# Optimization experiments

Hardware: AMD Instinct MI355X
Metric: run time of the kernel (lower is better)

Reference implementation:

```python
import jax, jax.numpy as jnp
import numpy as np

B, D, T = 16, 512, 2048
K, C = 8, 1024          # num_codebooks, codebook_size
CH = D // K             # chunk_size = 64
COMMIT = 0.25
EPS = 1e-8


def setup_inputs() -> dict:
    key = jax.random.key(0)
    k1, k2 = jax.random.split(key)
    x = jax.random.normal(k1, (B, D, T), dtype=jnp.float32)
    # kaiming-uniform-ish init for codebooks [K, C, CH]
    bound = float(np.sqrt(6.0 / CH))
    codebooks = jax.random.uniform(k2, (K, C, CH), dtype=jnp.float32,
                                   minval=-bound, maxval=bound)
    return {"x": x, "codebooks": codebooks}


def reference(x, codebooks):
    b, d, t = x.shape
    xc = x.reshape(b, K, CH, t)                       # [B,K,CH,T]
    x_norm = jnp.sum(xc * xc, axis=2)[:, :, None, :]  # [B,K,1,T]
    c_norm = jnp.sum(codebooks * codebooks, axis=2)[None, :, :, None]  # [1,K,C,1]
    cross = -2.0 * jnp.einsum('bkdt,kcd->bkct', xc, codebooks)         # [B,K,C,T]
    distances = x_norm + c_norm + cross
    indices = jnp.argmin(distances, axis=2)           # [B,K,T] int
    # gather nearest codewords -> [B,K,T,CH] -> [B,K,CH,T]
    q = codebooks[jnp.arange(K)[None, :, None], indices]
    q = jnp.transpose(q, (0, 1, 3, 2))                # [B,K,CH,T]
    # per-codebook usage histogram
    kk = jnp.broadcast_to(jnp.arange(K)[None, :, None], indices.shape)
    counts = jnp.zeros((K, C), dtype=jnp.float32).at[kk.ravel(), indices.ravel()].add(1.0)
    avg_probs = counts / (b * t)
    perplexity = jnp.exp(jnp.sum(-avg_probs * jnp.log(avg_probs + EPS), axis=1))
    # commitment losses
    sg = jax.lax.stop_gradient
    codebook_loss = jnp.mean((sg(xc) - q) ** 2)
    encoder_loss = jnp.mean((xc - sg(q)) ** 2)
    commit_loss = codebook_loss + COMMIT * encoder_loss
    # straight-through estimator
    quantized = xc + sg(q - xc)
    return quantized.reshape(b, d, t), commit_loss, perplexity
```

## Files before the change

kernel.cpp:

```cpp
#include <hip/hip_runtime.h>
#include <hip/hip_bf16.h>
#include <math.h>

#define B_   16
#define D_   512
#define T_   2048
#define K_   8
#define C_   1024
#define CH_  64
#define NEL_ (B_ * D_ * T_)
#define QOFF 16777216

#define WS_HCN   0
#define WS_CNT   32768
#define WS_SSE   65536
#define WS_CBS   66048

typedef __attribute__((ext_vector_type(8))) short   short8;
typedef __attribute__((ext_vector_type(8))) __bf16  bf16x8;
typedef __attribute__((ext_vector_type(4))) float   f32x4;

__device__ __forceinline__ unsigned short f2bf_rne(float f) {
    unsigned u = __builtin_bit_cast(unsigned, f);
    u = u + 0x7FFFu + ((u >> 16) & 1u);
    return (unsigned short)(u >> 16);
}

__device__ __forceinline__ void gload_lds16(const void* gsrc, void* ldst) {
    __builtin_amdgcn_global_load_lds(
        (const __attribute__((address_space(1))) unsigned int*)gsrc,
        (__attribute__((address_space(3))) unsigned int*)ldst,
        16, 0, 0);
}

__global__ void vq_prep(const float* __restrict__ cb,
                        unsigned char* __restrict__ cbS,
                        float* __restrict__ hcn,
                        int* __restrict__ counts,
                        double* __restrict__ sse) {
    int g   = blockIdx.x * 256 + threadIdx.x;
    if (g < K_ * C_) counts[g] = 0;
    if (g == 0) *sse = 0.0;

    int row = g >> 3;
    int s8  = g & 7;
    const float* src = cb + (size_t)row * CH_;

    short8 val;
#pragma unroll
    for (int j = 0; j < 8; ++j)
        val[j] = (short)f2bf_rne(-src[s8 * 8 + j]);
    *(short8*)(cbS + (size_t)row * 128 + ((s8 ^ (row & 7)) * 16)) = val;

    if (s8 == 0) {
        float s = 0.f;
#pragma unroll 8
        for (int ch = 0; ch < CH_; ++ch) {
            float v = src[ch];
            s = fmaf(v, v, s);
        }
        hcn[row] = 0.5f * s;
    }
}

#define LDSBUF 8192

__global__ __launch_bounds__(256, 8) void vq_main(
    const float* __restrict__ x,
    const float* __restrict__ cb,
    const unsigned char* __restrict__ cbS,
    const float* __restrict__ hcn,
    float* __restrict__ out,
    int* __restrict__ counts,
    double* __restrict__ sse)
{
    __shared__ __align__(16) unsigned char lds[2 * LDSBUF + 512];
    int* idxS = (int*)(lds + 2 * LDSBUF);

    const int tid  = threadIdx.x;
    const int lane = tid & 63;
    const int wave = tid >> 6;
    const int ln   = lane & 15;
    const int q    = lane >> 4;
    const int q4   = q * 4;

    const int bid = blockIdx.x;
    const int tc  = bid & 15;
    const int k   = (bid >> 4) & 7;
    const int b   = bid >> 7;
    const int t0  = tc * 128;
    const int tw  = t0 + wave * 32;

    short8 bh[2][2];
    float  xn[2];
#pragma unroll
    for (int tt = 0; tt < 2; ++tt) {
        int t = tw + tt * 16 + ln;
        float pn = 0.f;
#pragma unroll
        for (int ks = 0; ks < 2; ++ks) {
            const float* xp = x + ((size_t)(b * D_ + k * CH_ + ks * 32 + q * 8)) * T_ + t;
            short8 sh;
#pragma unroll
            for (int j = 0; j < 8; ++j) {
                float v = xp[(size_t)j * T_];
                pn = fmaf(v, v, pn);
                sh[j] = (short)f2bf_rne(v);
            }
            bh[tt][ks] = sh;
        }
        pn += __shfl_xor(pn, 16);
        pn += __shfl_xor(pn, 32);
        xn[tt] = pn;
    }

    const unsigned char* cbS_k = cbS + (size_t)k * C_ * 128;
    const float*         hcn_k = hcn + k * C_;

    {
        const unsigned char* src = cbS_k + tid * 16;
        unsigned char* dst = lds + tid * 16;
        gload_lds16(src,        dst);
        gload_lds16(src + 4096, dst + 4096);
    }

    float    md[2][4];
    unsigned mjp[2];
#pragma unroll
    for (int tt = 0; tt < 2; ++tt) {
        mjp[tt] = 0u;
#pragma unroll
        for (int r = 0; r < 4; ++r) md[tt][r] = INFINITY;
    }

    for (int chunk = 0; chunk < 16; ++chunk) {
        __syncthreads();

        if (chunk < 15) {
            const unsigned char* src = cbS_k + (size_t)(chunk + 1) * 8192 + tid * 16;
            unsigned char* dst = lds + ((chunk + 1) & 1) * LDSBUF + tid * 16;
            gload_lds16(src,        dst);
            gload_lds16(src + 4096, dst + 4096);
        }

        const unsigned char* buf = lds + (chunk & 1) * LDSBUF;
#pragma unroll
        for (int sub = 0; sub < 4; ++sub) {
            const unsigned char* rowb = buf + (sub * 16 + ln) * 128;
            f32x4 h4 = *(const f32x4*)(hcn_k + chunk * 64 + sub * 16 + q4);
            f32x4 a[2];
            a[0] = h4;
            a[1] = h4;
#pragma unroll
            for (int ks = 0; ks < 2; ++ks) {
                int cidx = ((ks * 4 + q) ^ (ln & 7)) * 16;
                bf16x8 ah = __builtin_bit_cast(bf16x8, *(const short8*)(rowb + cidx));
#pragma unroll
                for (int tt = 0; tt < 2; ++tt)
                    a[tt] = __builtin_amdgcn_mfma_f32_16x16x32_bf16(
                        ah, __builtin_bit_cast(bf16x8, bh[tt][ks]), a[tt], 0, 0, 0);
            }
            const unsigned j = (unsigned)(chunk * 4 + sub);
#pragma unroll
            for (int tt = 0; tt < 2; ++tt) {
#pragma unroll
                for (int r = 0; r < 4; ++r) {
                    bool lt = a[tt][r] < md[tt][r];
                    md[tt][r] = lt ? a[tt][r] : md[tt][r];
                    unsigned upd = (mjp[tt] & ~(0xFFu << (8 * r))) | (j << (8 * r));
                    mjp[tt] = lt ? upd : mjp[tt];
                }
            }
        }
    }

    double waveSse = 0.0;

#pragma unroll
    for (int tt = 0; tt < 2; ++tt) {
        float d1 = md[tt][0];
        int   c1 = (int)(mjp[tt] & 0xFFu) * 16 + q4;
#pragma unroll
        for (int r = 1; r < 4; ++r) {
            float v  = md[tt][r];
            int   cv = (int)((mjp[tt] >> (8 * r)) & 0xFFu) * 16 + q4 + r;
            bool w = (v < d1) || (v == d1 && cv < c1);
            d1 = w ? v : d1;
            c1 = w ? cv : c1;
        }
#pragma unroll
        for (int off = 16; off <= 32; off <<= 1) {
            float ov = __shfl_xor(d1, off);
            int   oc = __shfl_xor(c1, off);
            bool w = (ov < d1) || (ov == d1 && oc < c1);
            d1 = w ? ov : d1;
            c1 = w ? oc : c1;
        }

        if (q == 0) {
            waveSse += (double)(xn[tt] + 2.0f * d1);
            atomicAdd(&counts[k * C_ + c1], 1);
            idxS[wave * 32 + tt * 16 + ln] = c1;
        }
    }

    for (int off = 32; off > 0; off >>= 1) waveSse += __shfl_down(waveSse, off);
    if (lane == 0) atomicAdd(sse, waveSse);

    __syncthreads();

    const float* cb_k = cb + (size_t)k * C_ * CH_;
    const int i0 = idxS[2 * lane];
    const int i1 = idxS[2 * lane + 1];
    const float* r0 = cb_k + (size_t)i0 * CH_ + wave * 16;
    const float* r1 = cb_k + (size_t)i1 * CH_ + wave * 16;
#pragma unroll
    for (int p = 0; p < 4; ++p) {
        f32x4 a0 = *(const f32x4*)(r0 + 4 * p);
        f32x4 a1 = *(const f32x4*)(r1 + 4 * p);
#pragma unroll
        for (int jj = 0; jj < 4; ++jj) {
            int ch = wave * 16 + 4 * p + jj;
            float2 v = make_float2(a0[jj], a1[jj]);
            *(float2*)(out + ((size_t)(b * D_ + k * CH_ + ch)) * T_
                           + t0 + 2 * lane) = v;
        }
    }
}

__global__ void vq_final(const int* __restrict__ counts,
                         const double* __restrict__ sse,
                         float* __restrict__ out) {
    __shared__ double part[4];
    const int tid = threadIdx.x;
    const int k   = blockIdx.x;
    double local = 0.0;
    for (int j = tid; j < C_; j += 256) {
        double p = (double)counts[k * C_ + j] * (1.0 / (double)(B_ * T_));
        local += -p * log(p + 1e-8);
    }
    for (int off = 32; off > 0; off >>= 1) local += __shfl_down(local, off);
    if ((tid & 63) == 0) part[tid >> 6] = local;
    __syncthreads();
    if (tid == 0) {
        double sum = part[0] + part[1] + part[2] + part[3];
        out[QOFF + 1 + k] = (float)exp(sum);
        if (k == 0)
            out[QOFF] = (float)(1.25 * (*sse) / (double)NEL_);
    }
}

extern "C" void kernel_launch(void* const* d_in, const int* in_sizes, int n_in,
                              void* d_out, int out_size, void* d_ws, size_t ws_size,
                              hipStream_t stream) {
    const float* x  = (const float*)d_in[0];
    const float* cb = (const float*)d_in[1];
    float* out = (float*)d_out;

    float*         hcn    = (float*)((char*)d_ws + WS_HCN);
    int*           counts = (int*)((char*)d_ws + WS_CNT);
    double*        sse    = (double*)((char*)d_ws + WS_SSE);
    unsigned char* cbS    = (unsigned char*)((char*)d_ws + WS_CBS);

    vq_prep<<<(K_ * C_ * 8) / 256, 256, 0, stream>>>(cb, cbS, hcn, counts, sse);
    vq_main<<<B_ * K_ * (T_ / 128), 256, 0, stream>>>(x, cb, cbS, hcn,
                                                      out, counts, sse);
    vq_final<<<K_, 256, 0, stream>>>(counts, sse, out);
}
```

Measured before the change: 239.2 us.

## Read codebook directly from global memory and reduce argmin per tile

Removes the double-buffered LDS staging of the bf16 codebook, along with its per-chunk barriers and the XOR swizzle. Each wave now loads codebook fragments straight from global memory (relying on L1/L2 cache) inside an unrolled loop. The running argmin is also simplified to a single min and index per row-tile instead of four per lane, using fmin plus equality tests. The codebook is 128 KB per k, so this depends on cache hit rates and on the compiler overlapping global-load latency with MFMA work.

```diff
diff --git a/kernel.cpp b/kernel.cpp
--- a/kernel.cpp
+++ b/kernel.cpp
@@ -26,13 +26,6 @@
     return (unsigned short)(u >> 16);
 }
 
-__device__ __forceinline__ void gload_lds16(const void* gsrc, void* ldst) {
-    __builtin_amdgcn_global_load_lds(
-        (const __attribute__((address_space(1))) unsigned int*)gsrc,
-        (__attribute__((address_space(3))) unsigned int*)ldst,
-        16, 0, 0);
-}
-
 __global__ void vq_prep(const float* __restrict__ cb,
                         unsigned char* __restrict__ cbS,
                         float* __restrict__ hcn,
@@ -50,7 +43,7 @@
 #pragma unroll
     for (int j = 0; j < 8; ++j)
         val[j] = (short)f2bf_rne(-src[s8 * 8 + j]);
-    *(short8*)(cbS + (size_t)row * 128 + ((s8 ^ (row & 7)) * 16)) = val;
+    *(short8*)(cbS + (size_t)row * 128 + s8 * 16) = val;
 
     if (s8 == 0) {
         float s = 0.f;
@@ -62,8 +55,6 @@
         hcn[row] = 0.5f * s;
     }
 }
-
-#define LDSBUF 8192
 
 __global__ __launch_bounds__(256, 8) void vq_main(
     const float* __restrict__ x,
@@ -74,8 +65,7 @@
     int* __restrict__ counts,
     double* __restrict__ sse)
 {
-    __shared__ __align__(16) unsigned char lds[2 * LDSBUF + 512];
-    int* idxS = (int*)(lds + 2 * LDSBUF);
+    __shared__ int idxS[128];
 
     const int tid  = threadIdx.x;
     const int lane = tid & 63;
@@ -88,8 +78,8 @@
     const int tc  = bid & 15;
     const int k   = (bid >> 4) & 7;
     const int b   = bid >> 7;
-    const int t0  = tc * 128;
-    const int tw  = t0 + wave * 32;
+    const int t0b = tc * 128;
+    const int tw  = t0b + wave * 32;
 
     short8 bh[2][2];
     float  xn[2];
@@ -117,77 +107,47 @@
     const unsigned char* cbS_k = cbS + (size_t)k * C_ * 128;
     const float*         hcn_k = hcn + k * C_;
 
-    {
-        const unsigned char* src = cbS_k + tid * 16;
-        unsigned char* dst = lds + tid * 16;
-        gload_lds16(src,        dst);
-        gload_lds16(src + 4096, dst + 4096);
-    }
-
-    float    md[2][4];
-    unsigned mjp[2];
+    float md[2];
+    int   mc[2];
+#pragma unroll
+    for (int tt = 0; tt < 2; ++tt) { md[tt] = INFINITY; mc[tt] = 0; }
+
+#pragma unroll 4
+    for (int sub = 0; sub < 64; ++sub) {
+        const unsigned char* rowb = cbS_k + (size_t)((sub * 16 + ln) * 128);
+        f32x4 h4 = *(const f32x4*)(hcn_k + sub * 16 + q4);
+        f32x4 a[2];
+        a[0] = h4;
+        a[1] = h4;
+#pragma unroll
+        for (int ks = 0; ks < 2; ++ks) {
+            bf16x8 ah = __builtin_bit_cast(bf16x8,
+                            *(const short8*)(rowb + (ks * 4 + q) * 16));
+#pragma unroll
+            for (int tt = 0; tt < 2; ++tt)
+                a[tt] = __builtin_amdgcn_mfma_f32_16x16x32_bf16(
+                    ah, __builtin_bit_cast(bf16x8, bh[tt][ks]), a[tt], 0, 0, 0);
+        }
+        const int j4 = sub * 4;
+#pragma unroll
+        for (int tt = 0; tt < 2; ++tt) {
+            float m01 = fminf(a[tt][0], a[tt][1]);
+            float m23 = fminf(a[tt][2], a[tt][3]);
+            float m   = fminf(m01, m23);
+            int rw = (m == a[tt][0]) ? 0 :
+                     (m == a[tt][1]) ? 1 :
+                     (m == a[tt][2]) ? 2 : 3;
+            bool lt = m < md[tt];
+            md[tt] = lt ? m : md[tt];
+            mc[tt] = lt ? (j4 + rw) : mc[tt];
+        }
+    }
+
+    double waveSse = 0.0;
 #pragma unroll
     for (int tt = 0; tt < 2; ++tt) {
-        mjp[tt] = 0u;
-#pragma unroll
-        for (int r = 0; r < 4; ++r) md[tt][r] = INFINITY;
-    }
-
-    for (int chunk = 0; chunk < 16; ++chunk) {
-        __syncthreads();
-
-        if (chunk < 15) {
-            const unsigned char* src = cbS_k + (size_t)(chunk + 1) * 8192 + tid * 16;
-            unsigned char* dst = lds + ((chunk + 1) & 1) * LDSBUF + tid * 16;
-            gload_lds16(src,        dst);
-            gload_lds16(src + 4096, dst + 4096);
-        }
-
-        const unsigned char* buf = lds + (chunk & 1) * LDSBUF;
-#pragma unroll
-        for (int sub = 0; sub < 4; ++sub) {
-            const unsigned char* rowb = buf + (sub * 16 + ln) * 128;
-            f32x4 h4 = *(const f32x4*)(hcn_k + chunk * 64 + sub * 16 + q4);
-            f32x4 a[2];
-            a[0] = h4;
-            a[1] = h4;
-#pragma unroll
-            for (int ks = 0; ks < 2; ++ks) {
-                int cidx = ((ks * 4 + q) ^ (ln & 7)) * 16;
-                bf16x8 ah = __builtin_bit_cast(bf16x8, *(const short8*)(rowb + cidx));
-#pragma unroll
-                for (int tt = 0; tt < 2; ++tt)
-                    a[tt] = __builtin_amdgcn_mfma_f32_16x16x32_bf16(
-                        ah, __builtin_bit_cast(bf16x8, bh[tt][ks]), a[tt], 0, 0, 0);
-            }
-            const unsigned j = (unsigned)(chunk * 4 + sub);
-#pragma unroll
-            for (int tt = 0; tt < 2; ++tt) {
-#pragma unroll
-                for (int r = 0; r < 4; ++r) {
-                    bool lt = a[tt][r] < md[tt][r];
-                    md[tt][r] = lt ? a[tt][r] : md[tt][r];
-                    unsigned upd = (mjp[tt] & ~(0xFFu << (8 * r))) | (j << (8 * r));
-                    mjp[tt] = lt ? upd : mjp[tt];
-                }
-            }
-        }
-    }
-
-    double waveSse = 0.0;
-
-#pragma unroll
-    for (int tt = 0; tt < 2; ++tt) {
-        float d1 = md[tt][0];
-        int   c1 = (int)(mjp[tt] & 0xFFu) * 16 + q4;
-#pragma unroll
-        for (int r = 1; r < 4; ++r) {
-            float v  = md[tt][r];
-            int   cv = (int)((mjp[tt] >> (8 * r)) & 0xFFu) * 16 + q4 + r;
-            bool w = (v < d1) || (v == d1 && cv < c1);
-            d1 = w ? v : d1;
-            c1 = w ? cv : c1;
-        }
+        float d1 = md[tt];
+        int   c1 = ((mc[tt] >> 2) << 4) + q4 + (mc[tt] & 3);
 #pragma unroll
         for (int off = 16; off <= 32; off <<= 1) {
             float ov = __shfl_xor(d1, off);
@@ -223,7 +183,7 @@
             int ch = wave * 16 + 4 * p + jj;
             float2 v = make_float2(a0[jj], a1[jj]);
             *(float2*)(out + ((size_t)(b * D_ + k * CH_ + ch)) * T_
-                           + t0 + 2 * lane) = v;
+                           + t0b + 2 * lane) = v;
         }
     }
 }
```

New measurement: 311.9 us. +30.4%, slower.
